# Kernel optimization log

Hardware: AMD Instinct MI355X
Metric: run time of the kernel (lower is better)

Reference implementation:

```python
import jax, jax.numpy as jnp
import numpy as np

B, T, N = 8, 20, 256
BN = B * N
IN_DIM, H, HEADS, DH = 2, 128, 8, 16
FF = 4 * H
LAYERS = 5
EPS = 1e-5


def _ln(h, g, b):
    mu = h.mean(-1, keepdims=True)
    v = ((h - mu) ** 2).mean(-1, keepdims=True)
    return (h - mu) * jax.lax.rsqrt(v + EPS) * g + b


def setup_inputs() -> dict:
    key = jax.random.key(0)
    ks = jax.random.split(key, 16)
    ego_mask = jax.random.uniform(ks[0], (B, T, N)) > 0.2
    ego_mask = ego_mask.at[:, 0, :].set(True)  # every node active at t=0 (no fully-padded sequence)
    x_raw = jax.random.normal(ks[1], (T, BN, IN_DIM), dtype=jnp.float32)
    adj = (jax.random.uniform(ks[2], (T, BN, BN)) < 0.01).astype(jnp.float32)
    s = 0.02
    p = {}
    p['gcn1_w'] = jax.random.normal(ks[3], (IN_DIM, H), jnp.float32) * s
    p['gcn_ws'] = jax.random.normal(ks[4], (5, H, H), jnp.float32) * s
    p['gcn_bs'] = jnp.zeros((6, H), jnp.float32)
    p['ln_g'] = jnp.ones((6, H), jnp.float32)
    p['ln_b'] = jnp.zeros((6, H), jnp.float32)
    p['pos_embed'] = jax.random.normal(ks[5], (T, H), jnp.float32) * s
    p['t_wqkv'] = jax.random.normal(ks[6], (LAYERS, 3 * H, H), jnp.float32) * s
    p['t_bqkv'] = jnp.zeros((LAYERS, 3 * H), jnp.float32)
    p['t_wo'] = jax.random.normal(ks[7], (LAYERS, H, H), jnp.float32) * s
    p['t_bo'] = jnp.zeros((LAYERS, H), jnp.float32)
    p['t_ln1g'] = jnp.ones((LAYERS, H), jnp.float32)
    p['t_ln1b'] = jnp.zeros((LAYERS, H), jnp.float32)
    p['t_w1'] = jax.random.normal(ks[8], (LAYERS, FF, H), jnp.float32) * s
    p['t_b1'] = jnp.zeros((LAYERS, FF), jnp.float32)
    p['t_w2'] = jax.random.normal(ks[9], (LAYERS, H, FF), jnp.float32) * s
    p['t_b2'] = jnp.zeros((LAYERS, H), jnp.float32)
    p['t_ln2g'] = jnp.ones((LAYERS, H), jnp.float32)
    p['t_ln2b'] = jnp.zeros((LAYERS, H), jnp.float32)
    return dict(ego_mask=ego_mask, x_raw=x_raw, adj=adj, **p)


def _forward(ego_mask, x_raw, adj, gcn1_w, gcn_ws, gcn_bs, ln_g, ln_b, pos_embed,
             t_wqkv, t_bqkv, t_wo, t_bo, t_ln1g, t_ln1b, t_w1, t_b1, t_w2, t_b2,
             t_ln2g, t_ln2b):
    mask_flat = ego_mask.transpose(1, 0, 2).reshape(T, BN).astype(x_raw.dtype)  # [T, BN]

    def per_t(x_t, A_t, m):
        # masked subgraph + self-loops only on active nodes (PyG GCNConv on x[idx], A[idx][:,idx])
        Am = A_t * m[:, None] * m[None, :]
        Ahat = Am + jnp.diag(m)
        deg = Ahat.sum(0)                       # gcn_norm: degree at target (col of edge_index)
        dinv = jnp.where(deg > 0, jax.lax.rsqrt(deg), 0.0)
        S = (dinv[:, None] * Ahat * dinv[None, :]).T  # out[dst] = sum_src norm * x[src]

        def gcn(h, W, b):
            return S @ (h @ W) + b

        h = jax.nn.relu(_ln(gcn(x_t, gcn1_w, gcn_bs[0]), ln_g[0], ln_b[0]))
        for i in range(5):
            hr = _ln(gcn(h, gcn_ws[i], gcn_bs[i + 1]), ln_g[i + 1], ln_b[i + 1])
            h = jax.nn.relu(hr + h)  # residual then ReLU, as in source
        return h * m[:, None]        # inactive rows stay zero (x_placeholder)

    x_ph = jax.vmap(per_t)(x_raw, adj, mask_flat)          # [T, BN, H]
    x = x_ph.transpose(1, 0, 2) + pos_embed[None]          # [BN, T, H]

    # src_key_padding_mask: True = padded -> -inf on keys
    key_bias = jnp.where(mask_flat.T.astype(bool), 0.0, -jnp.inf)[:, None, None, :]  # [BN,1,1,T]
    scale = 1.0 / np.sqrt(DH)
    for l in range(LAYERS):  # post-norm TransformerEncoderLayer, activation=relu, eval (no dropout)
        qkv = x @ t_wqkv[l].T + t_bqkv[l]
        q, k, v = jnp.split(qkv, 3, axis=-1)
        q = q.reshape(BN, T, HEADS, DH)
        k = k.reshape(BN, T, HEADS, DH)
        v = v.reshape(BN, T, HEADS, DH)
        sc = jnp.einsum('bqhd,bkhd->bhqk', q, k) * scale + key_bias
        a = jax.nn.softmax(sc, axis=-1)
        o = jnp.einsum('bhqk,bkhd->bqhd', a, v).reshape(BN, T, H)
        o = o @ t_wo[l].T + t_bo[l]
        x = _ln(x + o, t_ln1g[l], t_ln1b[l])
        ff = jax.nn.relu(x @ t_w1[l].T + t_b1[l]) @ t_w2[l].T + t_b2[l]
        x = _ln(x + ff, t_ln2g[l], t_ln2b[l])
    return x.reshape(B, N, T, H)


def reference(ego_mask, x_raw, adj, gcn1_w, gcn_ws, gcn_bs, ln_g, ln_b, pos_embed,
              t_wqkv, t_bqkv, t_wo, t_bo, t_ln1g, t_ln1b, t_w1, t_b1, t_w2, t_b2,
              t_ln2g, t_ln2b):
    return _forward(ego_mask, x_raw, adj, gcn1_w, gcn_ws, gcn_bs, ln_g, ln_b,
                    pos_embed, t_wqkv, t_bqkv, t_wo, t_bo, t_ln1g, t_ln1b,
                    t_w1, t_b1, t_w2, t_b2, t_ln2g, t_ln2b)
```

## Files before the change

### kernel.cpp

```cpp
#include <hip/hip_runtime.h>
#include <hip/hip_bf16.h>
#include <cstdint>
#include <cstddef>

#define BNODES 2048
#define NT 20
#define HDIM 128
#define NROWS (NT * BNODES)
#define CAP 64

typedef __attribute__((ext_vector_type(8))) short short8;
typedef __attribute__((ext_vector_type(4))) float floatx4;

__device__ __forceinline__ float bf2f(short u) {
  return __uint_as_float(((unsigned int)(unsigned short)u) << 16);
}

__global__ void expand_mask_kernel(const void* __restrict__ ego, float* __restrict__ maskf,
                                   int* __restrict__ colcnt) {
  int gid = blockIdx.x * blockDim.x + threadIdx.x;
  if (gid >= NROWS) return;
  unsigned int w0 = ((const unsigned int*)ego)[0];
  int val;
  if (w0 == 1u)                 val = ((const int*)ego)[gid] != 0;
  else if (w0 == 0x3F800000u)   val = ((const float*)ego)[gid] != 0.0f;
  else if (w0 == 0x3F803F80u)   val = ((const unsigned short*)ego)[gid] != 0;
  else                          val = ((const unsigned char*)ego)[gid] != 0;
  int b = gid / (NT * 256);
  int t = (gid / 256) % NT;
  int n = gid % 256;
  maskf[t * BNODES + b * 256 + n] = val ? 1.0f : 0.0f;
  colcnt[gid] = 0;
}

__global__ __launch_bounds__(256) void build_edges_kernel(const float* __restrict__ adj,
                                                          const float* __restrict__ maskf,
                                                          int* __restrict__ colcnt,
                                                          int* __restrict__ colidx) {
  size_t e4 = (size_t)blockIdx.x * 256 + threadIdx.x;
  size_t e = e4 * 4;
  size_t row = e >> 11;
  if (maskf[row] == 0.0f) return;
  const float4 a = ((const float4*)adj)[e4];
  if (a.x == 0.0f && a.y == 0.0f && a.z == 0.0f && a.w == 0.0f) return;
  int i0 = (int)(e & (BNODES - 1));
  int t = (int)(row >> 11);
  int j = (int)(row & (BNODES - 1));
  int base = t * BNODES;
  if (a.x != 0.0f) { int p = atomicAdd(&colcnt[base + i0 + 0], 1); if (p < CAP) colidx[(size_t)(base + i0 + 0) * CAP + p] = j; }
  if (a.y != 0.0f) { int p = atomicAdd(&colcnt[base + i0 + 1], 1); if (p < CAP) colidx[(size_t)(base + i0 + 1) * CAP + p] = j; }
  if (a.z != 0.0f) { int p = atomicAdd(&colcnt[base + i0 + 2], 1); if (p < CAP) colidx[(size_t)(base + i0 + 2) * CAP + p] = j; }
  if (a.w != 0.0f) { int p = atomicAdd(&colcnt[base + i0 + 3], 1); if (p < CAP) colidx[(size_t)(base + i0 + 3) * CAP + p] = j; }
}

__global__ void finalize_deg_kernel(const float* __restrict__ maskf, int* __restrict__ colcnt,
                                    float* __restrict__ dinv) {
  int gid = blockIdx.x * blockDim.x + threadIdx.x;
  if (gid >= NROWS) return;
  int cnt = colcnt[gid];
  dinv[gid] = (maskf[gid] != 0.0f) ? rsqrtf((float)cnt + 1.0f) : 0.0f;
  colcnt[gid] = cnt < CAP ? cnt : CAP;
}

__global__ void conv_all_kernel(const float* __restrict__ a, const float* __restrict__ b,
                                const float* __restrict__ c, const float* __restrict__ d,
                                __hip_bfloat16* __restrict__ oa, __hip_bfloat16* __restrict__ ob,
                                __hip_bfloat16* __restrict__ oc, __hip_bfloat16* __restrict__ od) {
  int gid = blockIdx.x * blockDim.x + threadIdx.x;
  if (gid < 245760) { oa[gid] = __float2bfloat16(a[gid]); return; }
  gid -= 245760;
  if (gid < 81920) { ob[gid] = __float2bfloat16(b[gid]); return; }
  gid -= 81920;
  if (gid < 327680) { oc[gid] = __float2bfloat16(c[gid]); return; }
  gid -= 327680;
  od[gid] = __float2bfloat16(d[gid]);
}

__global__ void conv_t_bf16_kernel(const float* __restrict__ src, __hip_bfloat16* __restrict__ dst) {
  int gid = blockIdx.x * blockDim.x + threadIdx.x;
  if (gid >= 5 * 16384) return;
  int l = gid >> 14, rem = gid & 16383;
  int n = rem >> 7, k = rem & 127;
  dst[gid] = __float2bfloat16(src[(l << 14) + (k << 7) + n]);
}

__global__ __launch_bounds__(HDIM) void spmm_ln_kernel(const __hip_bfloat16* __restrict__ Y,
                                                       const float* __restrict__ xraw,
                                                       const float* __restrict__ gw,
                                                       const float* __restrict__ dinv,
                                                       const int* __restrict__ colcnt,
                                                       const int* __restrict__ colidx,
                                                       const float* __restrict__ bias,
                                                       const float* __restrict__ gamma,
                                                       const float* __restrict__ beta,
                                                       const float* __restrict__ resid,
                                                       const float* __restrict__ maskf,
                                                       const float* __restrict__ pos,
                                                       float* __restrict__ dstF,
                                                       __hip_bfloat16* __restrict__ dstB) {
  int r = blockIdx.x, c = threadIdx.x;
  int t = r >> 11;
  float di = dinv[r];
  float g0 = 0.0f, g1 = 0.0f;
  if (!Y) { g0 = gw[c]; g1 = gw[HDIM + c]; }
  float acc = 0.0f;
  if (di != 0.0f) {
    float yself = Y ? bf2f(((const short*)Y)[(size_t)r * HDIM + c])
                    : fmaf(xraw[2 * r], g0, xraw[2 * r + 1] * g1);
    acc = di * yself;
    int cnt = colcnt[r];
    const int* cols = colidx + (size_t)r * CAP;
    const float* dt = dinv + t * BNODES;
    for (int k = 0; k < cnt; ++k) {
      int j = cols[k];
      size_t gr = (size_t)t * BNODES + j;
      float yv = Y ? bf2f(((const short*)Y)[gr * HDIM + c])
                   : fmaf(xraw[2 * gr], g0, xraw[2 * gr + 1] * g1);
      acc = fmaf(dt[j], yv, acc);
    }
    acc *= di;
  }
  float v = acc + bias[c];
  float s = v, q = v * v;
  #pragma unroll
  for (int off = 32; off > 0; off >>= 1) {
    s += __shfl_down(s, off, 64);
    q += __shfl_down(q, off, 64);
  }
  __shared__ float ls[2], lq2[2];
  int wid = c >> 6, lane = c & 63;
  if (lane == 0) { ls[wid] = s; lq2[wid] = q; }
  __syncthreads();
  float mu = (ls[0] + ls[1]) * (1.0f / HDIM);
  float var = fmaxf((lq2[0] + lq2[1]) * (1.0f / HDIM) - mu * mu, 0.0f);
  float rs = rsqrtf(var + 1e-5f);
  float o = (v - mu) * rs * gamma[c] + beta[c];
  if (resid) o += resid[(size_t)r * HDIM + c];
  o = fmaxf(o, 0.0f);
  if (pos) {
    int bn = r & (BNODES - 1);
    float val = o * maskf[r] + pos[t * HDIM + c];
    size_t oi = ((size_t)bn * NT + t) * HDIM + c;
    dstF[oi] = val;
    dstB[oi] = __float2bfloat16(val);
  } else {
    size_t oi = (size_t)r * HDIM + c;
    dstF[oi] = o;
    dstB[oi] = __float2bfloat16(o);
  }
}

__device__ __forceinline__ void async16(const void* g, void* l) {
  __builtin_amdgcn_global_load_lds(
      (const __attribute__((address_space(1))) unsigned int*)g,
      (__attribute__((address_space(3))) unsigned int*)l, 16, 0, 0);
}

__global__ __launch_bounds__(256) void gemm_fused(const __hip_bfloat16* __restrict__ A,
                                                  const __hip_bfloat16* __restrict__ Bt,
                                                  const float* __restrict__ bias,
                                                  int K, int N, int relu,
                                                  float* __restrict__ Cf,
                                                  __hip_bfloat16* __restrict__ Cb,
                                                  const float* __restrict__ resid,
                                                  const float* __restrict__ lng,
                                                  const float* __restrict__ lnb,
                                                  float* __restrict__ lnF,
                                                  __hip_bfloat16* __restrict__ lnB) {
  __shared__ __align__(16) char smem[65536];
  __hip_bfloat16* As = (__hip_bfloat16*)smem;
  __hip_bfloat16* Bs = As + 128 * 128;
  float* Cs = (float*)smem;

  const int tid = threadIdx.x;
  const int wv = tid >> 6, ln = tid & 63;
  const int n0 = blockIdx.x << 7, m0 = blockIdx.y << 7;
  const int wm = (wv & 1) << 6, wn = (wv >> 1) << 6;
  const int lr = ln & 15, lq = ln >> 4;
  const int rsub = ln >> 4;
  const int slot = ln & 15;

  floatx4 acc[4][4];
  #pragma unroll
  for (int mi = 0; mi < 4; ++mi)
    #pragma unroll
    for (int ni = 0; ni < 4; ++ni) acc[mi][ni] = (floatx4)0.0f;

  for (int k0 = 0; k0 < K; k0 += 128) {
    if (k0) __syncthreads();
    #pragma unroll
    for (int i = 0; i < 8; ++i) {
      int rloc = i * 16 + wv * 4 + rsub;
      int sc = slot ^ (rloc & 15);
      async16((const char*)A + ((size_t)(m0 + rloc) * K + k0) * 2 + (size_t)sc * 16,
              (char*)As + (size_t)(i * 16 + wv * 4) * 256);
      async16((const char*)Bt + ((size_t)(n0 + rloc) * K + k0) * 2 + (size_t)sc * 16,
              (char*)Bs + (size_t)(i * 16 + wv * 4) * 256);
    }
    __syncthreads();
    #pragma unroll
    for (int kc = 0; kc < 4; ++kc) {
      short8 af[4], bfr[4];
      #pragma unroll
      for (int mi = 0; mi < 4; ++mi) {
        int R = wm + (mi << 4) + lr;
        int ch = ((kc << 2) + lq) ^ (R & 15);
        af[mi] = *(const short8*)(As + (R << 7) + (ch << 3));
      }
      #pragma unroll
      for (int ni = 0; ni < 4; ++ni) {
        int R = wn + (ni << 4) + lr;
        int ch = ((kc << 2) + lq) ^ (R & 15);
        bfr[ni] = *(const short8*)(Bs + (R << 7) + (ch << 3));
      }
      #pragma unroll
      for (int mi = 0; mi < 4; ++mi)
        #pragma unroll
        for (int ni = 0; ni < 4; ++ni)
          acc[mi][ni] = __builtin_amdgcn_mfma_f32_16x16x32_bf16(af[mi], bfr[ni], acc[mi][ni], 0, 0, 0);
    }
  }

  if (!lng) {
    #pragma unroll
    for (int ni = 0; ni < 4; ++ni) {
      int cn = n0 + wn + (ni << 4) + lr;
      float bv = bias ? bias[cn] : 0.0f;
      #pragma unroll
      for (int mi = 0; mi < 4; ++mi) {
        #pragma unroll
        for (int r = 0; r < 4; ++r) {
          int rm = m0 + wm + (mi << 4) + (lq << 2) + r;
          float v = acc[mi][ni][r] + bv;
          if (relu) v = fmaxf(v, 0.0f);
          size_t o = (size_t)rm * N + cn;
          if (Cf) Cf[o] = v;
          if (Cb) Cb[o] = __float2bfloat16(v);
        }
      }
    }
    return;
  }

  __syncthreads();
  #pragma unroll
  for (int ni = 0; ni < 4; ++ni) {
    int cn = wn + (ni << 4) + lr;
    float bv = bias[cn];
    #pragma unroll
    for (int mi = 0; mi < 4; ++mi) {
      #pragma unroll
      for (int r = 0; r < 4; ++r) {
        int rl = wm + (mi << 4) + (lq << 2) + r;
        float v = acc[mi][ni][r] + bv + resid[(size_t)(m0 + rl) * HDIM + cn];
        Cs[(rl << 7) + cn] = v;
      }
    }
  }
  __syncthreads();
  float2 gam = *(const float2*)(lng + ln * 2);
  float2 bet = *(const float2*)(lnb + ln * 2);
  #pragma unroll 4
  for (int p = 0; p < 32; ++p) {
    int rl = p * 4 + wv;
    float2 xv = *(const float2*)(Cs + (rl << 7) + ln * 2);
    float s = xv.x + xv.y, q = xv.x * xv.x + xv.y * xv.y;
    #pragma unroll
    for (int off = 32; off > 0; off >>= 1) {
      s += __shfl_xor(s, off, 64);
      q += __shfl_xor(q, off, 64);
    }
    float mu = s * (1.0f / HDIM);
    float var = fmaxf(q * (1.0f / HDIM) - mu * mu, 0.0f);
    float rs = rsqrtf(var + 1e-5f);
    float o0 = (xv.x - mu) * rs * gam.x + bet.x;
    float o1 = (xv.y - mu) * rs * gam.y + bet.y;
    size_t rowoff = (size_t)(m0 + rl) * HDIM;
    if (lnF) *(float2*)(lnF + rowoff + ln * 2) = make_float2(o0, o1);
    if (lnB) {
      __hip_bfloat16 b0 = __float2bfloat16(o0), b1 = __float2bfloat16(o1);
      unsigned int pk = ((unsigned int)*(unsigned short*)&b1 << 16) | *(unsigned short*)&b0;
      *(unsigned int*)((char*)lnB + (rowoff + ln * 2) * 2) = pk;
    }
  }
}

__global__ __launch_bounds__(256) void attn_kernel(const __hip_bfloat16* __restrict__ qkv,
                                                   const float* __restrict__ maskf,
                                                   __hip_bfloat16* __restrict__ o) {
  int bn = blockIdx.x;
  __shared__ float q[NT][HDIM], kk[NT][HDIM], vv[NT][HDIM];
  __shared__ float sc[8][NT][NT];
  int tid = threadIdx.x;
  for (int idx = tid; idx < NT * 48; idx += 256) {
    int t = idx / 48, c8 = idx % 48;
    short8 v8 = *(const short8*)((const short*)qkv + ((size_t)bn * NT + t) * 384 + c8 * 8);
    float* dst = (c8 < 16) ? &q[t][c8 * 8] : (c8 < 32) ? &kk[t][(c8 - 16) * 8] : &vv[t][(c8 - 32) * 8];
    #pragma unroll
    for (int i = 0; i < 8; ++i) dst[i] = bf2f(v8[i]);
  }
  __syncthreads();
  for (int idx = tid; idx < 8 * NT * NT; idx += 256) {
    int h = idx / (NT * NT), rr = idx % (NT * NT);
    int tq = rr / NT, tk = rr % NT;
    float s = 0.0f;
    #pragma unroll
    for (int d = 0; d < 16; ++d) s += q[tq][h * 16 + d] * kk[tk][h * 16 + d];
    s *= 0.25f;
    if (maskf[tk * BNODES + bn] == 0.0f) s = -1e30f;
    sc[h][tq][tk] = s;
  }
  __syncthreads();
  if (tid < 8 * NT) {
    int h = tid / NT, tq = tid % NT;
    float mx = -1e30f;
    for (int tk = 0; tk < NT; ++tk) mx = fmaxf(mx, sc[h][tq][tk]);
    float sum = 0.0f;
    for (int tk = 0; tk < NT; ++tk) { float e = __expf(sc[h][tq][tk] - mx); sc[h][tq][tk] = e; sum += e; }
    float inv = 1.0f / sum;
    for (int tk = 0; tk < NT; ++tk) sc[h][tq][tk] *= inv;
  }
  __syncthreads();
  for (int idx = tid; idx < NT * HDIM; idx += 256) {
    int tq = idx / HDIM, col = idx % HDIM;
    int h = col >> 4;
    float s = 0.0f;
    #pragma unroll
    for (int tk = 0; tk < NT; ++tk) s += sc[h][tq][tk] * vv[tk][col];
    o[((size_t)bn * NT + tq) * HDIM + col] = __float2bfloat16(s);
  }
}

extern "C" void kernel_launch(void* const* d_in, const int* in_sizes, int n_in,
                              void* d_out, int out_size, void* d_ws, size_t ws_size,
                              hipStream_t stream) {
  const void*  ego   = d_in[0];
  const float* xraw  = (const float*)d_in[1];
  const float* adj   = (const float*)d_in[2];
  const float* gcn1w = (const float*)d_in[3];
  const float* gcnws = (const float*)d_in[4];
  const float* gcnbs = (const float*)d_in[5];
  const float* lng   = (const float*)d_in[6];
  const float* lnb   = (const float*)d_in[7];
  const float* pos   = (const float*)d_in[8];
  const float* twqkv = (const float*)d_in[9];
  const float* tbqkv = (const float*)d_in[10];
  const float* two   = (const float*)d_in[11];
  const float* tbo   = (const float*)d_in[12];
  const float* tln1g = (const float*)d_in[13];
  const float* tln1b = (const float*)d_in[14];
  const float* tw1   = (const float*)d_in[15];
  const float* tb1   = (const float*)d_in[16];
  const float* tw2   = (const float*)d_in[17];
  const float* tb2   = (const float*)d_in[18];
  const float* tln2g = (const float*)d_in[19];
  const float* tln2b = (const float*)d_in[20];

  char* base = (char*)d_ws;
  size_t off = 0;
  auto alloc = [&](size_t bytes) -> void* {
    void* p = base + off;
    off = (off + bytes + 255) & ~(size_t)255;
    return p;
  };
  float* maskf  = (float*)alloc((size_t)NROWS * 4);
  float* dinv   = (float*)alloc((size_t)NROWS * 4);
  int*   colcnt = (int*)  alloc((size_t)NROWS * 4);
  void*  regA   = alloc((size_t)NROWS * 384 * 2);
  int*   colidx = (int*)regA;
  __hip_bfloat16* qkv_bf = (__hip_bfloat16*)regA;
  void*  regB   = alloc((size_t)NROWS * 512 * 2);
  __hip_bfloat16* t1_bf  = (__hip_bfloat16*)regB;
  __hip_bfloat16* big_bf = (__hip_bfloat16*)regB;
  void*  regC   = alloc((size_t)NROWS * HDIM * 2);
  __hip_bfloat16* hbuf_bf = (__hip_bfloat16*)regC;
  __hip_bfloat16* attn_bf = (__hip_bfloat16*)regC;
  float* hbuf   = (float*)alloc((size_t)NROWS * HDIM * 4);
  float* xbuf   = (float*)alloc((size_t)NROWS * HDIM * 4);
  __hip_bfloat16* xbf = (__hip_bfloat16*)alloc((size_t)NROWS * HDIM * 2);
  __hip_bfloat16* wqkv_bf = (__hip_bfloat16*)alloc((size_t)245760 * 2);
  __hip_bfloat16* wo_bf   = (__hip_bfloat16*)alloc((size_t)81920 * 2);
  __hip_bfloat16* w1_bf   = (__hip_bfloat16*)alloc((size_t)327680 * 2);
  __hip_bfloat16* w2_bf   = (__hip_bfloat16*)alloc((size_t)327680 * 2);
  __hip_bfloat16* wsT_bf  = (__hip_bfloat16*)alloc((size_t)81920 * 2);

  expand_mask_kernel<<<160, 256, 0, stream>>>(ego, maskf, colcnt);
  conv_all_kernel<<<3840, 256, 0, stream>>>(twqkv, two, tw1, tw2, wqkv_bf, wo_bf, w1_bf, w2_bf);
  conv_t_bf16_kernel<<<320, 256, 0, stream>>>(gcnws, wsT_bf);
  build_edges_kernel<<<81920, 256, 0, stream>>>(adj, maskf, colcnt, colidx);
  finalize_deg_kernel<<<160, 256, 0, stream>>>(maskf, colcnt, dinv);

  spmm_ln_kernel<<<NROWS, HDIM, 0, stream>>>(nullptr, xraw, gcn1w, dinv, colcnt, colidx,
                                             gcnbs, lng, lnb, nullptr, nullptr, nullptr,
                                             hbuf, hbuf_bf);
  for (int i = 0; i < 5; ++i) {
    gemm_fused<<<dim3(1, NROWS / 128), 256, 0, stream>>>(
        hbuf_bf, wsT_bf + (size_t)i * 16384, nullptr, 128, 128, 0,
        nullptr, t1_bf, nullptr, nullptr, nullptr, nullptr, nullptr);
    const float* fin_mask = (i == 4) ? maskf : nullptr;
    const float* fin_pos  = (i == 4) ? pos : nullptr;
    float* dF = (i == 4) ? xbuf : hbuf;
    __hip_bfloat16* dB = (i == 4) ? xbf : hbuf_bf;
    spmm_ln_kernel<<<NROWS, HDIM, 0, stream>>>(t1_bf, nullptr, nullptr, dinv, colcnt, colidx,
                                               gcnbs + (i + 1) * 128, lng + (i + 1) * 128,
                                               lnb + (i + 1) * 128, hbuf, fin_mask, fin_pos,
                                               dF, dB);
  }

  for (int l = 0; l < 5; ++l) {
    gemm_fused<<<dim3(3, NROWS / 128), 256, 0, stream>>>(
        xbf, wqkv_bf + (size_t)l * 49152, tbqkv + l * 384, 128, 384, 0,
        nullptr, qkv_bf, nullptr, nullptr, nullptr, nullptr, nullptr);
    attn_kernel<<<BNODES, 256, 0, stream>>>(qkv_bf, maskf, attn_bf);
    gemm_fused<<<dim3(1, NROWS / 128), 256, 0, stream>>>(
        attn_bf, wo_bf + (size_t)l * 16384, tbo + l * 128, 128, 128, 0,
        nullptr, nullptr, xbuf, tln1g + l * 128, tln1b + l * 128, xbuf, xbf);
    gemm_fused<<<dim3(4, NROWS / 128), 256, 0, stream>>>(
        xbf, w1_bf + (size_t)l * 65536, tb1 + l * 512, 128, 512, 1,
        nullptr, big_bf, nullptr, nullptr, nullptr, nullptr, nullptr);
    float* oF = (l == 4) ? (float*)d_out : xbuf;
    __hip_bfloat16* oB = (l == 4) ? nullptr : xbf;
    gemm_fused<<<dim3(1, NROWS / 128), 256, 0, stream>>>(
        big_bf, w2_bf + (size_t)l * 65536, tb2 + l * 128, 512, 128, 0,
        nullptr, nullptr, xbuf, tln2g + l * 128, tln2b + l * 128, oF, oB);
  }
}
```

Baseline: 1.758 ms.

## Reorder GCN to aggregate-then-transform, fuse GEMM with LN, split GEMM kernels

GCN layers now run the sparse aggregation first on the bf16 hidden state and then a GEMM whose epilogue applies bias, LayerNorm, residual, ReLU, mask and positional embedding. This replaces the separate per-row spmm+LN kernel that did the normalization after the dense transform. The single general GEMM is split into a plain kernel and an LN kernel, and the LN kernel uses 64-row tiles to double the number of blocks for N=128 outputs. The three setup kernels are merged into one launch. The reorder relies on A(XW)=(AX)W, so bf16 rounding now happens at a different point.

After: 1.655 ms. 1.06x faster.

```diff
diff --git a/kernel.cpp b/kernel.cpp
--- a/kernel.cpp
+++ b/kernel.cpp
@@ -16,21 +16,43 @@
   return __uint_as_float(((unsigned int)(unsigned short)u) << 16);
 }
 
-__global__ void expand_mask_kernel(const void* __restrict__ ego, float* __restrict__ maskf,
-                                   int* __restrict__ colcnt) {
+__global__ void setup_kernel(const void* __restrict__ ego, float* __restrict__ maskf,
+                             int* __restrict__ colcnt,
+                             const float* __restrict__ twqkv, const float* __restrict__ two,
+                             const float* __restrict__ tw1, const float* __restrict__ tw2,
+                             const float* __restrict__ gcnws,
+                             __hip_bfloat16* __restrict__ wqkv, __hip_bfloat16* __restrict__ wo,
+                             __hip_bfloat16* __restrict__ w1, __hip_bfloat16* __restrict__ w2,
+                             __hip_bfloat16* __restrict__ wsT) {
   int gid = blockIdx.x * blockDim.x + threadIdx.x;
-  if (gid >= NROWS) return;
-  unsigned int w0 = ((const unsigned int*)ego)[0];
-  int val;
-  if (w0 == 1u)                 val = ((const int*)ego)[gid] != 0;
-  else if (w0 == 0x3F800000u)   val = ((const float*)ego)[gid] != 0.0f;
-  else if (w0 == 0x3F803F80u)   val = ((const unsigned short*)ego)[gid] != 0;
-  else                          val = ((const unsigned char*)ego)[gid] != 0;
-  int b = gid / (NT * 256);
-  int t = (gid / 256) % NT;
-  int n = gid % 256;
-  maskf[t * BNODES + b * 256 + n] = val ? 1.0f : 0.0f;
-  colcnt[gid] = 0;
+  if (gid < NROWS) {
+    unsigned int w0 = ((const unsigned int*)ego)[0];
+    int val;
+    if (w0 == 1u)                 val = ((const int*)ego)[gid] != 0;
+    else if (w0 == 0x3F800000u)   val = ((const float*)ego)[gid] != 0.0f;
+    else if (w0 == 0x3F803F80u)   val = ((const unsigned short*)ego)[gid] != 0;
+    else                          val = ((const unsigned char*)ego)[gid] != 0;
+    int b = gid / (NT * 256);
+    int t = (gid / 256) % NT;
+    int n = gid % 256;
+    maskf[t * BNODES + b * 256 + n] = val ? 1.0f : 0.0f;
+    colcnt[gid] = 0;
+    return;
+  }
+  gid -= NROWS;
+  if (gid < 245760) { wqkv[gid] = __float2bfloat16(twqkv[gid]); return; }
+  gid -= 245760;
+  if (gid < 81920) { wo[gid] = __float2bfloat16(two[gid]); return; }
+  gid -= 81920;
+  if (gid < 327680) { w1[gid] = __float2bfloat16(tw1[gid]); return; }
+  gid -= 327680;
+  if (gid < 327680) { w2[gid] = __float2bfloat16(tw2[gid]); return; }
+  gid -= 327680;
+  if (gid < 81920) {
+    int l = gid >> 14, rem = gid & 16383;
+    int n = rem >> 7, k = rem & 127;
+    wsT[gid] = __float2bfloat16(gcnws[(l << 14) + (k << 7) + n]);
+  }
 }
 
 __global__ __launch_bounds__(256) void build_edges_kernel(const float* __restrict__ adj,
@@ -62,61 +84,30 @@
   colcnt[gid] = cnt < CAP ? cnt : CAP;
 }
 
-__global__ void conv_all_kernel(const float* __restrict__ a, const float* __restrict__ b,
-                                const float* __restrict__ c, const float* __restrict__ d,
-                                __hip_bfloat16* __restrict__ oa, __hip_bfloat16* __restrict__ ob,
-                                __hip_bfloat16* __restrict__ oc, __hip_bfloat16* __restrict__ od) {
-  int gid = blockIdx.x * blockDim.x + threadIdx.x;
-  if (gid < 245760) { oa[gid] = __float2bfloat16(a[gid]); return; }
-  gid -= 245760;
-  if (gid < 81920) { ob[gid] = __float2bfloat16(b[gid]); return; }
-  gid -= 81920;
-  if (gid < 327680) { oc[gid] = __float2bfloat16(c[gid]); return; }
-  gid -= 327680;
-  od[gid] = __float2bfloat16(d[gid]);
-}
-
-__global__ void conv_t_bf16_kernel(const float* __restrict__ src, __hip_bfloat16* __restrict__ dst) {
-  int gid = blockIdx.x * blockDim.x + threadIdx.x;
-  if (gid >= 5 * 16384) return;
-  int l = gid >> 14, rem = gid & 16383;
-  int n = rem >> 7, k = rem & 127;
-  dst[gid] = __float2bfloat16(src[(l << 14) + (k << 7) + n]);
-}
-
-__global__ __launch_bounds__(HDIM) void spmm_ln_kernel(const __hip_bfloat16* __restrict__ Y,
-                                                       const float* __restrict__ xraw,
-                                                       const float* __restrict__ gw,
-                                                       const float* __restrict__ dinv,
-                                                       const int* __restrict__ colcnt,
-                                                       const int* __restrict__ colidx,
-                                                       const float* __restrict__ bias,
-                                                       const float* __restrict__ gamma,
-                                                       const float* __restrict__ beta,
-                                                       const float* __restrict__ resid,
-                                                       const float* __restrict__ maskf,
-                                                       const float* __restrict__ pos,
-                                                       float* __restrict__ dstF,
-                                                       __hip_bfloat16* __restrict__ dstB) {
+__global__ __launch_bounds__(HDIM) void spmm_ln0_kernel(const float* __restrict__ xraw,
+                                                        const float* __restrict__ gw,
+                                                        const float* __restrict__ dinv,
+                                                        const int* __restrict__ colcnt,
+                                                        const int* __restrict__ colidx,
+                                                        const float* __restrict__ bias,
+                                                        const float* __restrict__ gamma,
+                                                        const float* __restrict__ beta,
+                                                        float* __restrict__ dstF,
+                                                        __hip_bfloat16* __restrict__ dstB) {
   int r = blockIdx.x, c = threadIdx.x;
   int t = r >> 11;
   float di = dinv[r];
-  float g0 = 0.0f, g1 = 0.0f;
-  if (!Y) { g0 = gw[c]; g1 = gw[HDIM + c]; }
+  float g0 = gw[c], g1 = gw[HDIM + c];
   float acc = 0.0f;
   if (di != 0.0f) {
-    float yself = Y ? bf2f(((const short*)Y)[(size_t)r * HDIM + c])
-                    : fmaf(xraw[2 * r], g0, xraw[2 * r + 1] * g1);
-    acc = di * yself;
+    acc = di * fmaf(xraw[2 * r], g0, xraw[2 * r + 1] * g1);
     int cnt = colcnt[r];
     const int* cols = colidx + (size_t)r * CAP;
     const float* dt = dinv + t * BNODES;
     for (int k = 0; k < cnt; ++k) {
       int j = cols[k];
       size_t gr = (size_t)t * BNODES + j;
-      float yv = Y ? bf2f(((const short*)Y)[gr * HDIM + c])
-                   : fmaf(xraw[2 * gr], g0, xraw[2 * gr + 1] * g1);
-      acc = fmaf(dt[j], yv, acc);
+      acc = fmaf(dt[j], fmaf(xraw[2 * gr], g0, xraw[2 * gr + 1] * g1), acc);
     }
     acc *= di;
   }
@@ -134,20 +125,33 @@
   float mu = (ls[0] + ls[1]) * (1.0f / HDIM);
   float var = fmaxf((lq2[0] + lq2[1]) * (1.0f / HDIM) - mu * mu, 0.0f);
   float rs = rsqrtf(var + 1e-5f);
-  float o = (v - mu) * rs * gamma[c] + beta[c];
-  if (resid) o += resid[(size_t)r * HDIM + c];
-  o = fmaxf(o, 0.0f);
-  if (pos) {
-    int bn = r & (BNODES - 1);
-    float val = o * maskf[r] + pos[t * HDIM + c];
-    size_t oi = ((size_t)bn * NT + t) * HDIM + c;
-    dstF[oi] = val;
-    dstB[oi] = __float2bfloat16(val);
-  } else {
-    size_t oi = (size_t)r * HDIM + c;
-    dstF[oi] = o;
-    dstB[oi] = __float2bfloat16(o);
-  }
+  float o = fmaxf((v - mu) * rs * gamma[c] + beta[c], 0.0f);
+  size_t oi = (size_t)r * HDIM + c;
+  dstF[oi] = o;
+  dstB[oi] = __float2bfloat16(o);
+}
+
+__global__ __launch_bounds__(HDIM) void spmm_kernel(const __hip_bfloat16* __restrict__ Y,
+                                                    const float* __restrict__ dinv,
+                                                    const int* __restrict__ colcnt,
+                                                    const int* __restrict__ colidx,
+                                                    __hip_bfloat16* __restrict__ out) {
+  int r = blockIdx.x, c = threadIdx.x;
+  int t = r >> 11;
+  float di = dinv[r];
+  size_t oi = (size_t)r * HDIM + c;
+  if (di == 0.0f) { out[oi] = __float2bfloat16(0.0f); return; }
+  const short* Ys = (const short*)Y;
+  float acc = di * bf2f(Ys[oi]);
+  int cnt = colcnt[r];
+  const int* cols = colidx + (size_t)r * CAP;
+  const float* dt = dinv + t * BNODES;
+  const short* Yt = Ys + (size_t)t * BNODES * HDIM;
+  for (int k = 0; k < cnt; ++k) {
+    int j = cols[k];
+    acc = fmaf(dt[j], bf2f(Yt[(size_t)j * HDIM + c]), acc);
+  }
+  out[oi] = __float2bfloat16(di * acc);
 }
 
 __device__ __forceinline__ void async16(const void* g, void* l) {
@@ -156,29 +160,19 @@
       (__attribute__((address_space(3))) unsigned int*)l, 16, 0, 0);
 }
 
-__global__ __launch_bounds__(256) void gemm_fused(const __hip_bfloat16* __restrict__ A,
+__global__ __launch_bounds__(256) void gemm_plain(const __hip_bfloat16* __restrict__ A,
                                                   const __hip_bfloat16* __restrict__ Bt,
                                                   const float* __restrict__ bias,
                                                   int K, int N, int relu,
-                                                  float* __restrict__ Cf,
-                                                  __hip_bfloat16* __restrict__ Cb,
-                                                  const float* __restrict__ resid,
-                                                  const float* __restrict__ lng,
-                                                  const float* __restrict__ lnb,
-                                                  float* __restrict__ lnF,
-                                                  __hip_bfloat16* __restrict__ lnB) {
+                                                  __hip_bfloat16* __restrict__ Cb) {
   __shared__ __align__(16) char smem[65536];
   __hip_bfloat16* As = (__hip_bfloat16*)smem;
   __hip_bfloat16* Bs = As + 128 * 128;
-  float* Cs = (float*)smem;
-
   const int tid = threadIdx.x;
   const int wv = tid >> 6, ln = tid & 63;
   const int n0 = blockIdx.x << 7, m0 = blockIdx.y << 7;
   const int wm = (wv & 1) << 6, wn = (wv >> 1) << 6;
   const int lr = ln & 15, lq = ln >> 4;
-  const int rsub = ln >> 4;
-  const int slot = ln & 15;
 
   floatx4 acc[4][4];
   #pragma unroll
@@ -190,8 +184,8 @@
     if (k0) __syncthreads();
     #pragma unroll
     for (int i = 0; i < 8; ++i) {
-      int rloc = i * 16 + wv * 4 + rsub;
-      int sc = slot ^ (rloc & 15);
+      int rloc = i * 16 + wv * 4 + lq;
+      int sc = (ln & 15) ^ (rloc & 15);
       async16((const char*)A + ((size_t)(m0 + rloc) * K + k0) * 2 + (size_t)sc * 16,
               (char*)As + (size_t)(i * 16 + wv * 4) * 256);
       async16((const char*)Bt + ((size_t)(n0 + rloc) * K + k0) * 2 + (size_t)sc * 16,
@@ -220,26 +214,88 @@
           acc[mi][ni] = __builtin_amdgcn_mfma_f32_16x16x32_bf16(af[mi], bfr[ni], acc[mi][ni], 0, 0, 0);
     }
   }
-
-  if (!lng) {
-    #pragma unroll
-    for (int ni = 0; ni < 4; ++ni) {
-      int cn = n0 + wn + (ni << 4) + lr;
-      float bv = bias ? bias[cn] : 0.0f;
-      #pragma unroll
-      for (int mi = 0; mi < 4; ++mi) {
+  #pragma unroll
+  for (int ni = 0; ni < 4; ++ni) {
+    int cn = n0 + wn + (ni << 4) + lr;
+    float bv = bias ? bias[cn] : 0.0f;
+    #pragma unroll
+    for (int mi = 0; mi < 4; ++mi) {
+      #pragma unroll
+      for (int r = 0; r < 4; ++r) {
+        int rm = m0 + wm + (mi << 4) + (lq << 2) + r;
+        float v = acc[mi][ni][r] + bv;
+        if (relu) v = fmaxf(v, 0.0f);
+        Cb[(size_t)rm * N + cn] = __float2bfloat16(v);
+      }
+    }
+  }
+}
+
+__global__ __launch_bounds__(256) void gemm_ln(const __hip_bfloat16* __restrict__ A,
+                                               const __hip_bfloat16* __restrict__ Bt,
+                                               const float* __restrict__ bias,
+                                               int K, int gcn_mode,
+                                               const float* __restrict__ resid,
+                                               const float* __restrict__ lng,
+                                               const float* __restrict__ lnb,
+                                               const float* __restrict__ maskf,
+                                               const float* __restrict__ pos,
+                                               float* __restrict__ outF,
+                                               __hip_bfloat16* __restrict__ outB) {
+  __shared__ __align__(16) char smem[49152];
+  __hip_bfloat16* As = (__hip_bfloat16*)smem;
+  __hip_bfloat16* Bs = As + 64 * 128;
+  float* Cs = (float*)smem;
+  const int tid = threadIdx.x;
+  const int wv = tid >> 6, ln = tid & 63;
+  const int m0 = blockIdx.x << 6;
+  const int wm = (wv & 1) << 5, wn = (wv >> 1) << 6;
+  const int lr = ln & 15, lq = ln >> 4;
+
+  floatx4 acc[2][4];
+  #pragma unroll
+  for (int mi = 0; mi < 2; ++mi)
+    #pragma unroll
+    for (int ni = 0; ni < 4; ++ni) acc[mi][ni] = (floatx4)0.0f;
+
+  for (int k0 = 0; k0 < K; k0 += 128) {
+    if (k0) __syncthreads();
+    #pragma unroll
+    for (int i = 0; i < 4; ++i) {
+      int rloc = i * 16 + wv * 4 + lq;
+      int sc = (ln & 15) ^ (rloc & 15);
+      async16((const char*)A + ((size_t)(m0 + rloc) * K + k0) * 2 + (size_t)sc * 16,
+              (char*)As + (size_t)(i * 16 + wv * 4) * 256);
+    }
+    #pragma unroll
+    for (int i = 0; i < 8; ++i) {
+      int rloc = i * 16 + wv * 4 + lq;
+      int sc = (ln & 15) ^ (rloc & 15);
+      async16((const char*)Bt + ((size_t)rloc * K + k0) * 2 + (size_t)sc * 16,
+              (char*)Bs + (size_t)(i * 16 + wv * 4) * 256);
+    }
+    __syncthreads();
+    #pragma unroll
+    for (int kc = 0; kc < 4; ++kc) {
+      short8 af[2], bfr[4];
+      #pragma unroll
+      for (int mi = 0; mi < 2; ++mi) {
+        int R = wm + (mi << 4) + lr;
+        int ch = ((kc << 2) + lq) ^ (R & 15);
+        af[mi] = *(const short8*)(As + (R << 7) + (ch << 3));
+      }
+      #pragma unroll
+      for (int ni = 0; ni < 4; ++ni) {
+        int R = wn + (ni << 4) + lr;
+        int ch = ((kc << 2) + lq) ^ (R & 15);
+        bfr[ni] = *(const short8*)(Bs + (R << 7) + (ch << 3));
+      }
+      #pragma unroll
+      for (int mi = 0; mi < 2; ++mi)
         #pragma unroll
-        for (int r = 0; r < 4; ++r) {
-          int rm = m0 + wm + (mi << 4) + (lq << 2) + r;
-          float v = acc[mi][ni][r] + bv;
-          if (relu) v = fmaxf(v, 0.0f);
-          size_t o = (size_t)rm * N + cn;
-          if (Cf) Cf[o] = v;
-          if (Cb) Cb[o] = __float2bfloat16(v);
-        }
-      }
-    }
-    return;
+        for (int ni = 0; ni < 4; ++ni)
+          acc[mi][ni] = __builtin_amdgcn_mfma_f32_16x16x32_bf16(af[mi], bfr[ni], acc[mi][ni], 0, 0, 0);
+    }
   }
 
   __syncthreads();
@@ -248,11 +304,12 @@
     int cn = wn + (ni << 4) + lr;
     float bv = bias[cn];
     #pragma unroll
-    for (int mi = 0; mi < 4; ++mi) {
+    for (int mi = 0; mi < 2; ++mi) {
       #pragma unroll
       for (int r = 0; r < 4; ++r) {
         int rl = wm + (mi << 4) + (lq << 2) + r;
-        float v = acc[mi][ni][r] + bv + resid[(size_t)(m0 + rl) * HDIM + cn];
+        float v = acc[mi][ni][r] + bv;
+        if (!gcn_mode) v += resid[(size_t)(m0 + rl) * HDIM + cn];
         Cs[(rl << 7) + cn] = v;
       }
     }
@@ -261,8 +318,9 @@
   float2 gam = *(const float2*)(lng + ln * 2);
   float2 bet = *(const float2*)(lnb + ln * 2);
   #pragma unroll 4
-  for (int p = 0; p < 32; ++p) {
+  for (int p = 0; p < 16; ++p) {
     int rl = p * 4 + wv;
+    int grow = m0 + rl;
     float2 xv = *(const float2*)(Cs + (rl << 7) + ln * 2);
     float s = xv.x + xv.y, q = xv.x * xv.x + xv.y * xv.y;
     #pragma unroll
@@ -275,12 +333,27 @@
     float rs = rsqrtf(var + 1e-5f);
     float o0 = (xv.x - mu) * rs * gam.x + bet.x;
     float o1 = (xv.y - mu) * rs * gam.y + bet.y;
-    size_t rowoff = (size_t)(m0 + rl) * HDIM;
-    if (lnF) *(float2*)(lnF + rowoff + ln * 2) = make_float2(o0, o1);
-    if (lnB) {
+    if (gcn_mode) {
+      float2 rv = *(const float2*)(resid + (size_t)grow * HDIM + ln * 2);
+      o0 = fmaxf(o0 + rv.x, 0.0f);
+      o1 = fmaxf(o1 + rv.y, 0.0f);
+    }
+    size_t oi;
+    if (pos) {
+      int t = grow >> 11, bn = grow & (BNODES - 1);
+      float m = maskf[grow];
+      float2 pv = *(const float2*)(pos + t * HDIM + ln * 2);
+      o0 = o0 * m + pv.x;
+      o1 = o1 * m + pv.y;
+      oi = ((size_t)bn * NT + t) * HDIM + ln * 2;
+    } else {
+      oi = (size_t)grow * HDIM + ln * 2;
+    }
+    if (outF) *(float2*)(outF + oi) = make_float2(o0, o1);
+    if (outB) {
       __hip_bfloat16 b0 = __float2bfloat16(o0), b1 = __float2bfloat16(o1);
       unsigned int pk = ((unsigned int)*(unsigned short*)&b1 << 16) | *(unsigned short*)&b0;
-      *(unsigned int*)((char*)lnB + (rowoff + ln * 2) * 2) = pk;
+      *(unsigned int*)((char*)outB + oi * 2) = pk;
     }
   }
 }
@@ -370,7 +443,7 @@
   int*   colidx = (int*)regA;
   __hip_bfloat16* qkv_bf = (__hip_bfloat16*)regA;
   void*  regB   = alloc((size_t)NROWS * 512 * 2);
-  __hip_bfloat16* t1_bf  = (__hip_bfloat16*)regB;
+  __hip_bfloat16* g_bf   = (__hip_bfloat16*)regB;
   __hip_bfloat16* big_bf = (__hip_bfloat16*)regB;
   void*  regC   = alloc((size_t)NROWS * HDIM * 2);
   __hip_bfloat16* hbuf_bf = (__hip_bfloat16*)regC;
@@ -384,44 +457,40 @@
   __hip_bfloat16* w2_bf   = (__hip_bfloat16*)alloc((size_t)327680 * 2);
   __hip_bfloat16* wsT_bf  = (__hip_bfloat16*)alloc((size_t)81920 * 2);
 
-  expand_mask_kernel<<<160, 256, 0, stream>>>(ego, maskf, colcnt);
-  conv_all_kernel<<<3840, 256, 0, stream>>>(twqkv, two, tw1, tw2, wqkv_bf, wo_bf, w1_bf, w2_bf);
-  conv_t_bf16_kernel<<<320, 256, 0, stream>>>(gcnws, wsT_bf);
+  setup_kernel<<<4320, 256, 0, stream>>>(ego, maskf, colcnt, twqkv, two, tw1, tw2, gcnws,
+                                         wqkv_bf, wo_bf, w1_bf, w2_bf, wsT_bf);
   build_edges_kernel<<<81920, 256, 0, stream>>>(adj, maskf, colcnt, colidx);
   finalize_deg_kernel<<<160, 256, 0, stream>>>(maskf, colcnt, dinv);
 
-  spmm_ln_kernel<<<NROWS, HDIM, 0, stream>>>(nullptr, xraw, gcn1w, dinv, colcnt, colidx,
-                                             gcnbs, lng, lnb, nullptr, nullptr, nullptr,
-                                             hbuf, hbuf_bf);
+  spmm_ln0_kernel<<<NROWS, HDIM, 0, stream>>>(xraw, gcn1w, dinv, colcnt, colidx,
+                                              gcnbs, lng, lnb, hbuf, hbuf_bf);
   for (int i = 0; i < 5; ++i) {
-    gemm_fused<<<dim3(1, NROWS / 128), 256, 0, stream>>>(
-        hbuf_bf, wsT_bf + (size_t)i * 16384, nullptr, 128, 128, 0,
-        nullptr, t1_bf, nullptr, nullptr, nullptr, nullptr, nullptr);
-    const float* fin_mask = (i == 4) ? maskf : nullptr;
-    const float* fin_pos  = (i == 4) ? pos : nullptr;
-    float* dF = (i == 4) ? xbuf : hbuf;
-    __hip_bfloat16* dB = (i == 4) ? xbf : hbuf_bf;
-    spmm_ln_kernel<<<NROWS, HDIM, 0, stream>>>(t1_bf, nullptr, nullptr, dinv, colcnt, colidx,
-                                               gcnbs + (i + 1) * 128, lng + (i + 1) * 128,
-                                               lnb + (i + 1) * 128, hbuf, fin_mask, fin_pos,
-                                               dF, dB);
+    spmm_kernel<<<NROWS, HDIM, 0, stream>>>(hbuf_bf, dinv, colcnt, colidx, g_bf);
+    const float* fm = (i == 4) ? maskf : nullptr;
+    const float* fp = (i == 4) ? pos : nullptr;
+    float* oF = (i == 4) ? xbuf : hbuf;
+    __hip_bfloat16* oB = (i == 4) ? xbf : hbuf_bf;
+    gemm_ln<<<NROWS / 64, 256, 0, stream>>>(g_bf, wsT_bf + (size_t)i * 16384,
+                                            gcnbs + (i + 1) * 128, 128, 1, hbuf,
+                                            lng + (i + 1) * 128, lnb + (i + 1) * 128,
+                                            fm, fp, oF, oB);
   }
 
   for (int l = 0; l < 5; ++l) {
-    gemm_fused<<<dim3(3, NROWS / 128), 256, 0, stream>>>(
-        xbf, wqkv_bf + (size_t)l * 49152, tbqkv + l * 384, 128, 384, 0,
-        nullptr, qkv_bf, nullptr, nullptr, nullptr, nullptr, nullptr);
+    gemm_plain<<<dim3(3, NROWS / 128), 256, 0, stream>>>(
+        xbf, wqkv_bf + (size_t)l * 49152, tbqkv + l * 384, 128, 384, 0, qkv_bf);
     attn_kernel<<<BNODES, 256, 0, stream>>>(qkv_bf, maskf, attn_bf);
-    gemm_fused<<<dim3(1, NROWS / 128), 256, 0, stream>>>(
-        attn_bf, wo_bf + (size_t)l * 16384, tbo + l * 128, 128, 128, 0,
-        nullptr, nullptr, xbuf, tln1g + l * 128, tln1b + l * 128, xbuf, xbf);
-    gemm_fused<<<dim3(4, NROWS / 128), 256, 0, stream>>>(
-        xbf, w1_bf + (size_t)l * 65536, tb1 + l * 512, 128, 512, 1,
-        nullptr, big_bf, nullptr, nullptr, nullptr, nullptr, nullptr);
+    gemm_ln<<<NROWS / 64, 256, 0, stream>>>(attn_bf, wo_bf + (size_t)l * 16384,
+                                            tbo + l * 128, 128, 0, xbuf,
+                                            tln1g + l * 128, tln1b + l * 128,
+                                            nullptr, nullptr, xbuf, xbf);
+    gemm_plain<<<dim3(4, NROWS / 128), 256, 0, stream>>>(
+        xbf, w1_bf + (size_t)l * 65536, tb1 + l * 512, 128, 512, 1, big_bf);
     float* oF = (l == 4) ? (float*)d_out : xbuf;
     __hip_bfloat16* oB = (l == 4) ? nullptr : xbf;
-    gemm_fused<<<dim3(1, NROWS / 128), 256, 0, stream>>>(
-        big_bf, w2_bf + (size_t)l * 65536, tb2 + l * 128, 512, 128, 0,
-        nullptr, nullptr, xbuf, tln2g + l * 128, tln2b + l * 128, oF, oB);
-  }
-}
+    gemm_ln<<<NROWS / 64, 256, 0, stream>>>(big_bf, w2_bf + (size_t)l * 65536,
+                                            tb2 + l * 128, 512, 0, xbuf,
+                                            tln2g + l * 128, tln2b + l * 128,
+                                            nullptr, nullptr, oF, oB);
+  }
+}
```
